# Optimization experiments

Measured on AMD Instinct MI355X. Metric: run time of the kernel, lower is better.

The kernel has to match this reference:

```python
import jax, jax.numpy as jnp
import numpy as np

NHEAD = 8
NEG_INF = -1e9
LN_EPS = 1e-5


def setup_inputs() -> dict:
    key = jax.random.key(0)
    ks = jax.random.split(key, 8)
    B, Q, N, C = 2, 256, 16384, 256
    return {
        "queries": jax.random.normal(ks[0], (B, Q, C), jnp.float32),
        "vid_features": jax.random.normal(ks[1], (B, C, N), jnp.float32),
        "vid_mask": jax.random.uniform(ks[2], (B, Q, N), jnp.float32),
        "pos_embed": jax.random.normal(ks[3], (B, C, N), jnp.float32),
        "query_embed": jax.random.normal(ks[4], (B, Q, C), jnp.float32),
        "in_proj_w": jax.random.normal(ks[5], (3 * C, C), jnp.float32) * 0.02,
        "in_proj_b": jnp.zeros((3 * C,), jnp.float32),
        "out_proj_w": jax.random.normal(ks[6], (C, C), jnp.float32) * 0.02,
        "out_proj_b": jnp.zeros((C,), jnp.float32),
        "ln_gamma": jnp.ones((C,), jnp.float32),
        "ln_beta": jnp.zeros((C,), jnp.float32),
    }


def reference(queries, vid_features, vid_mask, pos_embed, query_embed,
              in_proj_w, in_proj_b, out_proj_w, out_proj_b, ln_gamma, ln_beta):
    B, Q, C = queries.shape
    H = NHEAD
    d = C // H

    vf = jnp.transpose(vid_features, (0, 2, 1))   # B N C
    pe = jnp.transpose(pos_embed, (0, 2, 1))      # B N C

    q_in = queries + query_embed                  # with_pos_embed on queries
    k_in = vf + pe                                # with_pos_embed on keys
    v_in = vf

    wq, wk, wv = jnp.split(in_proj_w, 3, axis=0)
    bq, bk, bv = jnp.split(in_proj_b, 3)

    q = (q_in @ wq.T + bq).reshape(B, Q, H, d)
    k = (k_in @ wk.T + bk).reshape(B, -1, H, d)
    v = (v_in @ wv.T + bv).reshape(B, -1, H, d)

    scale = 1.0 / jnp.sqrt(jnp.asarray(d, q.dtype))
    logits = jnp.einsum('bqhd,bnhd->bhqn', q, k) * scale  # B H Q N

    # Hard masking: block keys where mask prob < 0.5; if a query row is
    # fully blocked, fall back to unmasked attention (avoid NaN softmax).
    blocked = vid_mask < 0.5                                 # B Q N
    all_blocked = jnp.all(blocked, axis=-1, keepdims=True)   # B Q 1
    blocked = blocked & jnp.logical_not(all_blocked)
    logits = jnp.where(blocked[:, None, :, :], NEG_INF, logits)

    attn = jax.nn.softmax(logits, axis=-1)
    ctx = jnp.einsum('bhqn,bnhd->bqhd', attn, v).reshape(B, Q, C)
    tgt2 = ctx @ out_proj_w.T + out_proj_b

    # residual + LayerNorm (dropout p=0.0 -> identity)
    x = queries + tgt2
    mu = jnp.mean(x, axis=-1, keepdims=True)
    var = jnp.mean(jnp.square(x - mu), axis=-1, keepdims=True)
    return (x - mu) / jnp.sqrt(var + LN_EPS) * ln_gamma + ln_beta
```

## Files before the change

kernel.cpp:

```cpp
#include <hip/hip_runtime.h>
#include <stdint.h>

#define B_ 2
#define Q_ 256
#define N_ 16384
#define C_ 256
#define H_ 8
#define D_ 32
#define NC_ 32
#define SCALEQ 0.2550542176432015f

typedef __bf16 bf16x8 __attribute__((ext_vector_type(8)));
typedef float f32x4 __attribute__((ext_vector_type(4)));

__device__ __forceinline__ uint16_t bfbits(float f) {
  union { __bf16 h; uint16_t u; } c; c.h = (__bf16)f; return c.u;
}
__device__ __forceinline__ float bf2f(uint16_t u) {
  union { uint32_t u; float f; } c; c.u = (uint32_t)u << 16;
  return c.f;
}
__device__ __forceinline__ uint32_t pk2(float a, float b) {
  union { struct { uint16_t lo, hi; } s; uint32_t u; } c;
  c.s.lo = bfbits(a); c.s.hi = bfbits(b);
  return c.u;
}
__device__ __forceinline__ void lgkm0_barrier() {
  __builtin_amdgcn_sched_barrier(0);
  asm volatile("s_waitcnt lgkmcnt(0)" ::: "memory");
  __builtin_amdgcn_sched_barrier(0);
  __builtin_amdgcn_s_barrier();
  __builtin_amdgcn_sched_barrier(0);
}

__global__ __launch_bounds__(256) void prep(const float* __restrict__ inw,
                                            const float* __restrict__ outw,
                                            const float* __restrict__ vm,
                                            uint16_t* __restrict__ wb,
                                            float* __restrict__ woT,
                                            uint32_t* __restrict__ mb) {
  __shared__ __align__(16) char sh[4352];
  const int bid = blockIdx.x;
  const int t = threadIdx.x;
  if (bid < 96) {
    const int i = (bid * 256 + t) * 8;
    const float4 a = *reinterpret_cast<const float4*>(inw + i);
    const float4 b = *reinterpret_cast<const float4*>(inw + i + 4);
    ushort4 lo = {bfbits(a.x), bfbits(a.y), bfbits(a.z), bfbits(a.w)};
    ushort4 hi = {bfbits(b.x), bfbits(b.y), bfbits(b.z), bfbits(b.w)};
    *reinterpret_cast<ushort4*>(wb + i) = lo;
    *reinterpret_cast<ushort4*>(wb + i + 4) = hi;
  } else if (bid < 160) {
    float(*s)[33] = reinterpret_cast<float(*)[33]>(sh);
    const int bb = bid - 96;
    const int bx = bb & 7, by = bb >> 3;
    const int r0 = by * 32, c0 = bx * 32;
    const int tr = t >> 5, tc = t & 31;
#pragma unroll
    for (int k = 0; k < 4; ++k)
      s[tr + 8 * k][tc] = outw[(size_t)(r0 + tr + 8 * k) * 256 + c0 + tc];
    __syncthreads();
#pragma unroll
    for (int k = 0; k < 4; ++k)
      woT[(size_t)(c0 + tr + 8 * k) * 256 + r0 + tc] = s[tc][tr + 8 * k];
  } else {
    uint8_t(*nib)[256] = reinterpret_cast<uint8_t(*)[256]>(sh);
    __shared__ int wcnt[4];
    __shared__ int tot;
    const int bq = bid - 160;
    const float* row = vm + (size_t)bq * N_;
    const int lane = t & 63;
    int cnt = 0;
#pragma unroll
    for (int i = 0; i < 16; ++i) {
      const float4 v = *reinterpret_cast<const float4*>(&row[i * 1024 + 4 * t]);
      const uint32_t nb = (v.x < 0.5f ? 1u : 0u) | (v.y < 0.5f ? 2u : 0u) |
                          (v.z < 0.5f ? 4u : 0u) | (v.w < 0.5f ? 8u : 0u);
      nib[i][t] = (uint8_t)nb;
      cnt += __popc(nb);
    }
    for (int o = 32; o > 0; o >>= 1) cnt += __shfl_down(cnt, o, 64);
    if (lane == 0) wcnt[t >> 6] = cnt;
    __syncthreads();
    if (t == 0) tot = wcnt[0] + wcnt[1] + wcnt[2] + wcnt[3];
    __syncthreads();
    const bool allb = (tot == N_);
    uint32_t* dst = mb + (size_t)bq * 512;
#pragma unroll
    for (int k = 0; k < 2; ++k) {
      const int w = k * 256 + t;
      const int i = w >> 5, tw = w & 31;
      const uint2 u = *reinterpret_cast<const uint2*>(&nib[i][8 * tw]);
      uint32_t y0 = u.x & 0x0F0F0F0Fu; y0 = y0 | (y0 >> 4);
      uint32_t y1 = u.y & 0x0F0F0F0Fu; y1 = y1 | (y1 >> 4);
      const uint32_t word = (y0 & 0xFFu) | (((y0 >> 16) & 0xFFu) << 8) |
                            ((y1 & 0xFFu) << 16) | (((y1 >> 16) & 0xFFu) << 24);
      dst[w] = allb ? 0u : word;
    }
  }
}

__global__ __launch_bounds__(512, 2) void kvqproj(const float* __restrict__ vf,
                                                  const float* __restrict__ pe,
                                                  const float* __restrict__ queries,
                                                  const float* __restrict__ qembed,
                                                  const uint16_t* __restrict__ wkv,
                                                  const float* __restrict__ bias,
                                                  uint16_t* __restrict__ Kh,
                                                  uint16_t* __restrict__ Vh,
                                                  uint16_t* __restrict__ Qb) {
  __shared__ __align__(16) uint16_t shpool[8][64][40];
  const int bid = blockIdx.x;
  const int t = threadIdx.x, wid = t >> 6, lane = t & 63;
  const int g = lane >> 4, c15 = lane & 15;

  if (bid >= 8) {
    const int kb = bid - 8;
    const int b = kb >> 8, nt = kb & 255;
    const int n0 = nt * 64;
    const int w = wid;

    const uint16_t* WsecK = wkv + (size_t)(256 + w * 32 + c15) * C_;
    const uint16_t* WsecV = wkv + (size_t)(512 + w * 32 + c15) * C_;

    f32x4 acck[8];
    f32x4 accv[8];
#pragma unroll
    for (int cf = 0; cf < 2; ++cf) {
      f32x4 ivk;
#pragma unroll
      for (int j = 0; j < 4; ++j) ivk[j] = bias[256 + w * 32 + cf * 16 + 4 * g + j];
      const float bv = bias[512 + w * 32 + cf * 16 + c15];
      const f32x4 ivv = {bv, bv, bv, bv};
#pragma unroll
      for (int nf = 0; nf < 4; ++nf) {
        acck[cf * 4 + nf] = ivk;
        accv[nf * 2 + cf] = ivv;
      }
    }

    const int cq = t >> 5, q2 = t & 31;
    const float* Xb = vf + ((size_t)b * C_ + 2 * cq) * N_ + n0 + 2 * q2;
    const float* Pb = pe + ((size_t)b * C_ + 2 * cq) * N_ + n0 + 2 * q2;
    const int cqs = cq ^ (((q2 >> 2) & 3) << 2);

    float2 xA0, xA1, pA0, pA1, xB0, xB1, pB0, pB1;
    bf16x8 Wk[2], Wv[2];

#define LOADW(s)                                                             \
    {                                                                        \
      _Pragma("unroll") for (int cf = 0; cf < 2; ++cf) {                     \
        Wk[cf] = *(const bf16x8*)(WsecK + (size_t)cf * 16 * C_ + (s) * 32 + g * 8); \
        Wv[cf] = *(const bf16x8*)(WsecV + (size_t)cf * 16 * C_ + (s) * 32 + g * 8); \
      }                                                                      \
    }
#define LOADA(X0, X1, P0, P1, s)                                             \
    {                                                                        \
      const float* x_ = Xb + (size_t)(s) * 32 * N_;                          \
      const float* p_ = Pb + (size_t)(s) * 32 * N_;                          \
      X0 = *(const float2*)x_;                                               \
      X1 = *(const float2*)(x_ + N_);                                        \
      P0 = *(const float2*)p_;                                               \
      P1 = *(const float2*)(p_ + N_);                                        \
    }
#define WRITEA(X0, X1, P0, P1, bufp)                                         \
    {                                                                        \
      *(uint32_t*)&shpool[bufp][2 * q2][2 * cqs]     = pk2(X0.x + P0.x, X1.x + P1.x); \
      *(uint32_t*)&shpool[bufp][2 * q2 + 1][2 * cqs] = pk2(X0.y + P0.y, X1.y + P1.y); \
      *(uint32_t*)&shpool[(bufp) + 1][2 * q2][2 * cqs]     = pk2(X0.x, X1.x); \
      *(uint32_t*)&shpool[(bufp) + 1][2 * q2 + 1][2 * cqs] = pk2(X0.y, X1.y); \
    }
#define COMPUTE(bufp)                                                        \
    {                                                                        \
      _Pragma("unroll") for (int nf = 0; nf < 4; ++nf) {                     \
        const int r_ = nf * 16 + c15;                                        \
        const int o_ = (g ^ ((r_ >> 3) & 3)) * 8;                            \
        const bf16x8 Fp = *(const bf16x8*)&shpool[bufp][r_][o_];             \
        const bf16x8 Fv = *(const bf16x8*)&shpool[(bufp) + 1][r_][o_];       \
        _Pragma("unroll") for (int cf = 0; cf < 2; ++cf) {                   \
          acck[cf * 4 + nf] = __builtin_amdgcn_mfma_f32_16x16x32_bf16(       \
              Wk[cf], Fp, acck[cf * 4 + nf], 0, 0, 0);                       \
          accv[nf * 2 + cf] = __builtin_amdgcn_mfma_f32_16x16x32_bf16(       \
              Fv, Wv[cf], accv[nf * 2 + cf], 0, 0, 0);                       \
        }                                                                    \
      }                                                                      \
    }

    LOADA(xA0, xA1, pA0, pA1, 0);
    LOADA(xB0, xB1, pB0, pB1, 1);
    LOADW(0); WRITEA(xA0, xA1, pA0, pA1, 0); LOADA(xA0, xA1, pA0, pA1, 2);
    lgkm0_barrier(); COMPUTE(0); __builtin_amdgcn_sched_barrier(0);
    LOADW(1); WRITEA(xB0, xB1, pB0, pB1, 2); LOADA(xB0, xB1, pB0, pB1, 3);
    lgkm0_barrier(); COMPUTE(2); __builtin_amdgcn_sched_barrier(0);
    LOADW(2); WRITEA(xA0, xA1, pA0, pA1, 0); LOADA(xA0, xA1, pA0, pA1, 4);
    lgkm0_barrier(); COMPUTE(0); __builtin_amdgcn_sched_barrier(0);
    LOADW(3); WRITEA(xB0, xB1, pB0, pB1, 2); LOADA(xB0, xB1, pB0, pB1, 5);
    lgkm0_barrier(); COMPUTE(2); __builtin_amdgcn_sched_barrier(0);
    LOADW(4); WRITEA(xA0, xA1, pA0, pA1, 0); LOADA(xA0, xA1, pA0, pA1, 6);
    lgkm0_barrier(); COMPUTE(0); __builtin_amdgcn_sched_barrier(0);
    LOADW(5); WRITEA(xB0, xB1, pB0, pB1, 2); LOADA(xB0, xB1, pB0, pB1, 7);
    lgkm0_barrier(); COMPUTE(2); __builtin_amdgcn_sched_barrier(0);
    LOADW(6); WRITEA(xA0, xA1, pA0, pA1, 0);
    lgkm0_barrier(); COMPUTE(0); __builtin_amdgcn_sched_barrier(0);
    LOADW(7); WRITEA(xB0, xB1, pB0, pB1, 2);
    lgkm0_barrier(); COMPUTE(2); __builtin_amdgcn_sched_barrier(0);

#undef LOADW
#undef LOADA
#undef WRITEA
#undef COMPUTE

    uint16_t* Kp = Kh + (size_t)(b * H_ + w) * N_ * D_;
#pragma unroll
    for (int cf = 0; cf < 2; ++cf)
#pragma unroll
      for (int nf = 0; nf < 4; ++nf) {
        const f32x4 a = acck[cf * 4 + nf];
        uint2 pkv;
        pkv.x = pk2(a[0], a[1]);
        pkv.y = pk2(a[2], a[3]);
        *(uint2*)&Kp[(size_t)(n0 + nf * 16 + c15) * D_ + cf * 16 + 4 * g] = pkv;
      }
    uint16_t* Vp = Vh + (size_t)(b * H_ + w) * D_ * N_;
#pragma unroll
    for (int nf = 0; nf < 4; ++nf)
#pragma unroll
      for (int cf = 0; cf < 2; ++cf) {
        const f32x4 a = accv[nf * 2 + cf];
        uint2 pkv;
        pkv.x = pk2(a[0], a[1]);
        pkv.y = pk2(a[2], a[3]);
        *(uint2*)&Vp[(size_t)(cf * 16 + c15) * N_ + n0 + nf * 16 + 4 * g] = pkv;
      }
  } else {
    const int qb = bid;
    const int q0g = qb * 64;
    const int b = q0g >> 8, q0 = q0g & 255;
    const int r = t >> 3, c0 = (t & 7) * 32, s = t & 7;
    const float* Qrow = queries + (size_t)(q0g + r) * C_ + c0;
    const float* Erow = qembed + (size_t)(q0g + r) * C_ + c0;
#pragma unroll
    for (int ph = 0; ph < 2; ++ph) {
      float4 a4[4], e4[4];
#pragma unroll
      for (int k = 0; k < 4; ++k) a4[k] = reinterpret_cast<const float4*>(Qrow + ph * 16)[k];
#pragma unroll
      for (int k = 0; k < 4; ++k) e4[k] = reinterpret_cast<const float4*>(Erow + ph * 16)[k];
      const float* af = reinterpret_cast<const float*>(a4);
      const float* ef = reinterpret_cast<const float*>(e4);
#pragma unroll
      for (int i = 0; i < 16; ++i) {
        const int cl = ph * 16 + i;
        const int col = cl ^ (8 * ((r >> 3) & 3));
        shpool[s][r][col] = bfbits(af[i] + ef[i]);
      }
      __builtin_amdgcn_sched_barrier(0);
    }
    lgkm0_barrier();

    const int w = wid;
    f32x4 acc[4][2];
#pragma unroll
    for (int nf = 0; nf < 2; ++nf) {
      const float bv = bias[w * 32 + nf * 16 + c15];
      const f32x4 iv = {bv, bv, bv, bv};
#pragma unroll
      for (int qf = 0; qf < 4; ++qf) acc[qf][nf] = iv;
    }
#pragma unroll
    for (int s8 = 0; s8 < 8; ++s8) {
      bf16x8 Bf[2];
#pragma unroll
      for (int nf = 0; nf < 2; ++nf)
        Bf[nf] = *reinterpret_cast<const bf16x8*>(
            wkv + (size_t)(w * 32 + nf * 16 + c15) * C_ + s8 * 32 + g * 8);
#pragma unroll
      for (int qf = 0; qf < 4; ++qf) {
        const int rr = qf * 16 + c15;
        const bf16x8 Af = *reinterpret_cast<const bf16x8*>(
            &shpool[s8][rr][8 * (g ^ ((rr >> 3) & 3))]);
#pragma unroll
        for (int nf = 0; nf < 2; ++nf)
          acc[qf][nf] = __builtin_amdgcn_mfma_f32_16x16x32_bf16(Af, Bf[nf], acc[qf][nf], 0, 0, 0);
      }
    }
#pragma unroll
    for (int qf = 0; qf < 4; ++qf)
#pragma unroll
      for (int nf = 0; nf < 2; ++nf)
#pragma unroll
        for (int j = 0; j < 4; ++j) {
          const int q = q0 + qf * 16 + 4 * g + j;
          const int dk = nf * 16 + c15;
          Qb[((size_t)(b * H_ + w) * Q_ + q) * D_ + dk] = bfbits(acc[qf][nf][j] * SCALEQ);
        }
  }
}

__global__ __launch_bounds__(512) void attn(const uint16_t* __restrict__ Qb,
                                            const uint16_t* __restrict__ Kh,
                                            const uint16_t* __restrict__ Vh,
                                            const uint32_t* __restrict__ mb,
                                            uint16_t* __restrict__ ctx_part,
                                            float* __restrict__ lsum_part) {
  const int bid = blockIdx.x;
  const int nc = bid & 31, h = (bid >> 5) & 7, b = bid >> 8;
  const int t = threadIdx.x, wid = t >> 6, lane = t & 63;
  const int g = lane >> 4, c15 = lane & 15;
  const int qw0 = wid * 32;
  const int nbase = nc * (N_ / NC_);
  constexpr int SS = (N_ / NC_) / 128;

  __shared__ __align__(16) uint16_t kst[2][128][40];
  __shared__ __align__(16) uint16_t vst[2][32][136];
  __shared__ __align__(16) uint16_t plds[8][32][40];

  const uint16_t* Qp = Qb + (size_t)(b * H_ + h) * Q_ * D_;
  bf16x8 qfr[2];
#pragma unroll
  for (int qf = 0; qf < 2; ++qf)
    qfr[qf] = *reinterpret_cast<const bf16x8*>(Qp + (size_t)(qw0 + qf * 16 + c15) * D_ + g * 8);

  f32x4 acc[2][2];
  const f32x4 zero4 = {0.f, 0.f, 0.f, 0.f};
#pragma unroll
  for (int qf = 0; qf < 2; ++qf)
#pragma unroll
    for (int dvf = 0; dvf < 2; ++dvf) acc[qf][dvf] = zero4;
  float lsum[2][4] = {};

  const uint32_t* mrow = mb + (size_t)b * Q_ * (N_ / 32);

  const int krow = t >> 2, kch = t & 3;
  const uint16_t* ksrc = Kh + ((size_t)(b * H_ + h) * N_ + nbase + krow) * 32 + kch * 8;
  const int vrow = t >> 4, vch = t & 15;
  const uint16_t* vsrc = Vh + ((size_t)(b * H_ + h) * 32 + vrow) * N_ + nbase + vch * 8;

  uint4 kreg = *(const uint4*)ksrc;
  uint4 vreg = *(const uint4*)vsrc;

  int cur = 0;
  for (int ss = 0; ss < SS; ++ss) {
    *(uint4*)&kst[cur][krow][kch * 8] = kreg;
    *(uint4*)&vst[cur][vrow][vch * 8] = vreg;
    if (ss < SS - 1) {
      kreg = *(const uint4*)(ksrc + (size_t)(ss + 1) * 128 * 32);
      vreg = *(const uint4*)(vsrc + (ss + 1) * 128);
    }
    lgkm0_barrier();

    const int nstart = nbase + ss * 128;
#pragma unroll
    for (int half = 0; half < 2; ++half) {
      uint32_t mw[2][4][2];
#pragma unroll
      for (int qf = 0; qf < 2; ++qf)
#pragma unroll
        for (int j = 0; j < 4; ++j) {
          const int q = qw0 + qf * 16 + 4 * g + j;
          const uint2 u = *reinterpret_cast<const uint2*>(
              &mrow[(size_t)q * (N_ / 32) + (nstart >> 5) + half * 2]);
          mw[qf][j][0] = u.x;
          mw[qf][j][1] = u.y;
        }
#pragma unroll
      for (int s2 = 0; s2 < 2; ++s2) {
        const int sub = half * 2 + s2;
        const int nl0 = sub * 32;
        bf16x8 kfr[2];
#pragma unroll
        for (int nf = 0; nf < 2; ++nf)
          kfr[nf] = *reinterpret_cast<const bf16x8*>(&kst[cur][nl0 + nf * 16 + c15][g * 8]);
        f32x4 s[2][2];
#pragma unroll
        for (int qf = 0; qf < 2; ++qf)
#pragma unroll
          for (int nf = 0; nf < 2; ++nf)
            s[qf][nf] = __builtin_amdgcn_mfma_f32_16x16x32_bf16(qfr[qf], kfr[nf], zero4, 0, 0, 0);

#pragma unroll
        for (int qf = 0; qf < 2; ++qf) {
#pragma unroll
          for (int j = 0; j < 4; ++j) {
            const uint32_t wmask = mw[qf][j][s2];
#pragma unroll
            for (int nf = 0; nf < 2; ++nf) {
              const int bit = nf * 16 + c15;
              const float p = ((wmask >> bit) & 1u) ? 0.0f : exp2f(s[qf][nf][j]);
              lsum[qf][j] += p;
              plds[wid][qf * 16 + 4 * g + j][nf * 16 + c15] = bfbits(p);
            }
          }
        }
        __asm__ volatile("s_waitcnt lgkmcnt(0)" ::: "memory");
#pragma unroll
        for (int qf = 0; qf < 2; ++qf) {
          const bf16x8 pa = *reinterpret_cast<const bf16x8*>(&plds[wid][qf * 16 + c15][g * 8]);
#pragma unroll
          for (int dvf = 0; dvf < 2; ++dvf) {
            const bf16x8 vb =
                *reinterpret_cast<const bf16x8*>(&vst[cur][dvf * 16 + c15][nl0 + g * 8]);
            acc[qf][dvf] = __builtin_amdgcn_mfma_f32_16x16x32_bf16(pa, vb, acc[qf][dvf], 0, 0, 0);
          }
        }
      }
    }
    __builtin_amdgcn_sched_barrier(0);
    cur ^= 1;
  }

#pragma unroll
  for (int qf = 0; qf < 2; ++qf)
#pragma unroll
    for (int j = 0; j < 4; ++j) {
      float v = lsum[qf][j];
      v += __shfl_xor(v, 1, 64);
      v += __shfl_xor(v, 2, 64);
      v += __shfl_xor(v, 4, 64);
      v += __shfl_xor(v, 8, 64);
      lsum[qf][j] = v;
    }

#pragma unroll
  for (int qf = 0; qf < 2; ++qf)
#pragma unroll
    for (int dvf = 0; dvf < 2; ++dvf)
#pragma unroll
      for (int j = 0; j < 4; ++j) {
        const int q = qw0 + qf * 16 + 4 * g + j;
        const size_t base = (((size_t)(b * Q_ + q) * H_ + h) * NC_ + nc) * D_;
        ctx_part[base + dvf * 16 + c15] = bfbits(acc[qf][dvf][j]);
      }
  if (c15 == 0) {
#pragma unroll
    for (int qf = 0; qf < 2; ++qf)
#pragma unroll
      for (int j = 0; j < 4; ++j) {
        const int q = qw0 + qf * 16 + 4 * g + j;
        lsum_part[((size_t)(b * Q_ + q) * H_ + h) * NC_ + nc] = lsum[qf][j];
      }
  }
}

__global__ __launch_bounds__(256) void epilogue(const uint16_t* __restrict__ ctx_part,
                                                const float* __restrict__ lsum_part,
                                                const float* __restrict__ queries,
                                                const float* __restrict__ woT,
                                                const float* __restrict__ bo,
                                                const float* __restrict__ gamma,
                                                const float* __restrict__ beta,
                                                float* __restrict__ out) {
  const int bq = blockIdx.x;
  const int t = threadIdx.x;
  const int h = t >> 5, dv = t & 31;
  const uint16_t* crow = ctx_part + (size_t)bq * H_ * NC_ * D_;
  const float* lrow = lsum_part + (size_t)bq * H_ * NC_;
  float cs = 0.f, ls = 0.f;
#pragma unroll 8
  for (int k = 0; k < NC_; ++k) {
    cs += bf2f(crow[((size_t)h * NC_ + k) * D_ + dv]);
    ls += lrow[h * NC_ + k];
  }
  __shared__ float ctxrow[C_];
  ctxrow[t] = cs / ls;
  __syncthreads();
  float acc = bo[t];
#pragma unroll 8
  for (int j = 0; j < C_; ++j) acc = fmaf(ctxrow[j], woT[(size_t)j * C_ + t], acc);
  const float x = queries[(size_t)bq * C_ + t] + acc;
  float s1 = x, s2 = x * x;
  for (int o = 32; o > 0; o >>= 1) {
    s1 += __shfl_down(s1, o, 64);
    s2 += __shfl_down(s2, o, 64);
  }
  __shared__ float r1[4], r2[4];
  if ((t & 63) == 0) { r1[t >> 6] = s1; r2[t >> 6] = s2; }
  __syncthreads();
  const float mu = (r1[0] + r1[1] + r1[2] + r1[3]) * (1.0f / C_);
  const float e2 = (r2[0] + r2[1] + r2[2] + r2[3]) * (1.0f / C_);
  const float var = e2 - mu * mu;
  out[(size_t)bq * C_ + t] = (x - mu) * rsqrtf(var + 1e-5f) * gamma[t] + beta[t];
}

extern "C" void kernel_launch(void* const* d_in, const int* in_sizes, int n_in,
                              void* d_out, int out_size, void* d_ws, size_t ws_size,
                              hipStream_t stream) {
  const float* queries    = (const float*)d_in[0];
  const float* vidfeat    = (const float*)d_in[1];
  const float* vidmask    = (const float*)d_in[2];
  const float* posembed   = (const float*)d_in[3];
  const float* queryembed = (const float*)d_in[4];
  const float* inw        = (const float*)d_in[5];
  const float* inb        = (const float*)d_in[6];
  const float* outw       = (const float*)d_in[7];
  const float* outb       = (const float*)d_in[8];
  const float* gamma      = (const float*)d_in[9];
  const float* beta       = (const float*)d_in[10];
  float* out = (float*)d_out;

  char* ws = (char*)d_ws;
  size_t off = 0;
  uint16_t* Qb   = (uint16_t*)(ws + off); off += (size_t)B_ * H_ * Q_ * D_ * 2;
  uint16_t* Kh   = (uint16_t*)(ws + off); off += (size_t)B_ * H_ * N_ * D_ * 2;
  uint16_t* Vh   = (uint16_t*)(ws + off); off += (size_t)B_ * H_ * D_ * N_ * 2;
  uint32_t* mb   = (uint32_t*)(ws + off); off += (size_t)B_ * Q_ * (N_ / 32) * 4;
  uint16_t* wkv  = (uint16_t*)(ws + off); off += (size_t)768 * C_ * 2;
  float* woT     = (float*)(ws + off);    off += (size_t)C_ * C_ * 4;
  uint16_t* ctxp = (uint16_t*)(ws + off); off += (size_t)B_ * Q_ * H_ * NC_ * D_ * 2;
  float* lsump   = (float*)(ws + off);    off += (size_t)B_ * Q_ * H_ * NC_ * 4;

  prep<<<dim3(672), dim3(256), 0, stream>>>(inw, outw, vidmask, wkv, woT, mb);
  kvqproj<<<dim3(520), dim3(512), 0, stream>>>(vidfeat, posembed, queries, queryembed,
                                               wkv, inb, Kh, Vh, Qb);
  attn<<<dim3(B_ * H_ * NC_), dim3(512), 0, stream>>>(Qb, Kh, Vh, mb, ctxp, lsump);
  epilogue<<<dim3(B_ * Q_), dim3(256), 0, stream>>>(ctxp, lsump, queries, woT, outb,
                                                    gamma, beta, out);
}
```

Baseline: 94.67 us.

## Split K and V projection across separate waves with 128-row tiles in 1024-thread blocks

The K/V projection block grows from 512 to 1024 threads and from 64 to 128 sequence rows. Waves 0-7 compute K and waves 8-15 compute V, so each wave holds one accumulator set and one weight fragment instead of both. The aim is to lower per-wave register pressure and to double the reuse of the staged activation tile. In exchange the grid shrinks to 264 blocks, which may under-fill the GPU, and half the threads sit idle in the Q-projection blocks.

```diff
diff --git a/kernel.cpp b/kernel.cpp
--- a/kernel.cpp
+++ b/kernel.cpp
@@ -100,59 +100,61 @@
   }
 }
 
-__global__ __launch_bounds__(512, 2) void kvqproj(const float* __restrict__ vf,
-                                                  const float* __restrict__ pe,
-                                                  const float* __restrict__ queries,
-                                                  const float* __restrict__ qembed,
-                                                  const uint16_t* __restrict__ wkv,
-                                                  const float* __restrict__ bias,
-                                                  uint16_t* __restrict__ Kh,
-                                                  uint16_t* __restrict__ Vh,
-                                                  uint16_t* __restrict__ Qb) {
-  __shared__ __align__(16) uint16_t shpool[8][64][40];
+__global__ __launch_bounds__(1024, 4) void kvqproj(const float* __restrict__ vf,
+                                                   const float* __restrict__ pe,
+                                                   const float* __restrict__ queries,
+                                                   const float* __restrict__ qembed,
+                                                   const uint16_t* __restrict__ wkv,
+                                                   const float* __restrict__ bias,
+                                                   uint16_t* __restrict__ Kh,
+                                                   uint16_t* __restrict__ Vh,
+                                                   uint16_t* __restrict__ Qb) {
+  __shared__ __align__(16) uint16_t shp[2][2][128][40];
   const int bid = blockIdx.x;
   const int t = threadIdx.x, wid = t >> 6, lane = t & 63;
   const int g = lane >> 4, c15 = lane & 15;
 
   if (bid >= 8) {
     const int kb = bid - 8;
-    const int b = kb >> 8, nt = kb & 255;
-    const int n0 = nt * 64;
-    const int w = wid;
-
-    const uint16_t* WsecK = wkv + (size_t)(256 + w * 32 + c15) * C_;
-    const uint16_t* WsecV = wkv + (size_t)(512 + w * 32 + c15) * C_;
-
-    f32x4 acck[8];
-    f32x4 accv[8];
-#pragma unroll
-    for (int cf = 0; cf < 2; ++cf) {
-      f32x4 ivk;
-#pragma unroll
-      for (int j = 0; j < 4; ++j) ivk[j] = bias[256 + w * 32 + cf * 16 + 4 * g + j];
-      const float bv = bias[512 + w * 32 + cf * 16 + c15];
-      const f32x4 ivv = {bv, bv, bv, bv};
-#pragma unroll
-      for (int nf = 0; nf < 4; ++nf) {
-        acck[cf * 4 + nf] = ivk;
-        accv[nf * 2 + cf] = ivv;
-      }
-    }
-
-    const int cq = t >> 5, q2 = t & 31;
-    const float* Xb = vf + ((size_t)b * C_ + 2 * cq) * N_ + n0 + 2 * q2;
-    const float* Pb = pe + ((size_t)b * C_ + 2 * cq) * N_ + n0 + 2 * q2;
-    const int cqs = cq ^ (((q2 >> 2) & 3) << 2);
+    const int b = kb >> 7, nt = kb & 127;
+    const int n0 = nt * 128;
+    const bool isK = wid < 8;
+    const int w = wid & 7;
+
+    const uint16_t* Wsec = wkv + (size_t)((isK ? 256 : 512) + w * 32 + c15) * C_;
+
+    f32x4 acc[16];
+    if (isK) {
+#pragma unroll
+      for (int cf = 0; cf < 2; ++cf) {
+        f32x4 iv;
+#pragma unroll
+        for (int j = 0; j < 4; ++j) iv[j] = bias[256 + w * 32 + cf * 16 + 4 * g + j];
+#pragma unroll
+        for (int nf = 0; nf < 8; ++nf) acc[cf * 8 + nf] = iv;
+      }
+    } else {
+#pragma unroll
+      for (int cf = 0; cf < 2; ++cf) {
+        const float bv = bias[512 + w * 32 + cf * 16 + c15];
+        const f32x4 iv = {bv, bv, bv, bv};
+#pragma unroll
+        for (int nf = 0; nf < 8; ++nf) acc[nf * 2 + cf] = iv;
+      }
+    }
+
+    const int cp = t >> 6, n2 = lane;
+    const float* Xb = vf + ((size_t)b * C_ + 2 * cp) * N_ + n0 + 2 * n2;
+    const float* Pb = pe + ((size_t)b * C_ + 2 * cp) * N_ + n0 + 2 * n2;
+    const int cps = cp ^ (((n2 >> 2) & 3) << 2);
 
     float2 xA0, xA1, pA0, pA1, xB0, xB1, pB0, pB1;
-    bf16x8 Wk[2], Wv[2];
+    bf16x8 W[2];
 
 #define LOADW(s)                                                             \
     {                                                                        \
-      _Pragma("unroll") for (int cf = 0; cf < 2; ++cf) {                     \
-        Wk[cf] = *(const bf16x8*)(WsecK + (size_t)cf * 16 * C_ + (s) * 32 + g * 8); \
-        Wv[cf] = *(const bf16x8*)(WsecV + (size_t)cf * 16 * C_ + (s) * 32 + g * 8); \
-      }                                                                      \
+      _Pragma("unroll") for (int cf = 0; cf < 2; ++cf)                       \
+          W[cf] = *(const bf16x8*)(Wsec + (size_t)cf * 16 * C_ + (s) * 32 + g * 8); \
     }
 #define LOADA(X0, X1, P0, P1, s)                                             \
     {                                                                        \
@@ -163,25 +165,28 @@
       P0 = *(const float2*)p_;                                               \
       P1 = *(const float2*)(p_ + N_);                                        \
     }
-#define WRITEA(X0, X1, P0, P1, bufp)                                         \
+#define WRITEA(X0, X1, P0, P1, buf)                                          \
     {                                                                        \
-      *(uint32_t*)&shpool[bufp][2 * q2][2 * cqs]     = pk2(X0.x + P0.x, X1.x + P1.x); \
-      *(uint32_t*)&shpool[bufp][2 * q2 + 1][2 * cqs] = pk2(X0.y + P0.y, X1.y + P1.y); \
-      *(uint32_t*)&shpool[(bufp) + 1][2 * q2][2 * cqs]     = pk2(X0.x, X1.x); \
-      *(uint32_t*)&shpool[(bufp) + 1][2 * q2 + 1][2 * cqs] = pk2(X0.y, X1.y); \
-    }
-#define COMPUTE(bufp)                                                        \
+      *(uint32_t*)&shp[0][buf][2 * n2][2 * cps]     = pk2(X0.x + P0.x, X1.x + P1.x); \
+      *(uint32_t*)&shp[0][buf][2 * n2 + 1][2 * cps] = pk2(X0.y + P0.y, X1.y + P1.y); \
+      *(uint32_t*)&shp[1][buf][2 * n2][2 * cps]     = pk2(X0.x, X1.x);       \
+      *(uint32_t*)&shp[1][buf][2 * n2 + 1][2 * cps] = pk2(X0.y, X1.y);       \
+    }
+#define COMPUTE(buf)                                                         \
     {                                                                        \
-      _Pragma("unroll") for (int nf = 0; nf < 4; ++nf) {                     \
+      _Pragma("unroll") for (int nf = 0; nf < 8; ++nf) {                     \
         const int r_ = nf * 16 + c15;                                        \
         const int o_ = (g ^ ((r_ >> 3) & 3)) * 8;                            \
-        const bf16x8 Fp = *(const bf16x8*)&shpool[bufp][r_][o_];             \
-        const bf16x8 Fv = *(const bf16x8*)&shpool[(bufp) + 1][r_][o_];       \
-        _Pragma("unroll") for (int cf = 0; cf < 2; ++cf) {                   \
-          acck[cf * 4 + nf] = __builtin_amdgcn_mfma_f32_16x16x32_bf16(       \
-              Wk[cf], Fp, acck[cf * 4 + nf], 0, 0, 0);                       \
-          accv[nf * 2 + cf] = __builtin_amdgcn_mfma_f32_16x16x32_bf16(       \
-              Fv, Wv[cf], accv[nf * 2 + cf], 0, 0, 0);                       \
+        if (isK) {                                                           \
+          const bf16x8 Fp = *(const bf16x8*)&shp[0][buf][r_][o_];            \
+          _Pragma("unroll") for (int cf = 0; cf < 2; ++cf)                   \
+              acc[cf * 8 + nf] = __builtin_amdgcn_mfma_f32_16x16x32_bf16(    \
+                  W[cf], Fp, acc[cf * 8 + nf], 0, 0, 0);                     \
+        } else {                                                             \
+          const bf16x8 Fv = *(const bf16x8*)&shp[1][buf][r_][o_];            \
+          _Pragma("unroll") for (int cf = 0; cf < 2; ++cf)                   \
+              acc[nf * 2 + cf] = __builtin_amdgcn_mfma_f32_16x16x32_bf16(    \
+                  Fv, W[cf], acc[nf * 2 + cf], 0, 0, 0);                     \
         }                                                                    \
       }                                                                      \
     }
@@ -190,110 +195,117 @@
     LOADA(xB0, xB1, pB0, pB1, 1);
     LOADW(0); WRITEA(xA0, xA1, pA0, pA1, 0); LOADA(xA0, xA1, pA0, pA1, 2);
     lgkm0_barrier(); COMPUTE(0); __builtin_amdgcn_sched_barrier(0);
-    LOADW(1); WRITEA(xB0, xB1, pB0, pB1, 2); LOADA(xB0, xB1, pB0, pB1, 3);
-    lgkm0_barrier(); COMPUTE(2); __builtin_amdgcn_sched_barrier(0);
+    LOADW(1); WRITEA(xB0, xB1, pB0, pB1, 1); LOADA(xB0, xB1, pB0, pB1, 3);
+    lgkm0_barrier(); COMPUTE(1); __builtin_amdgcn_sched_barrier(0);
     LOADW(2); WRITEA(xA0, xA1, pA0, pA1, 0); LOADA(xA0, xA1, pA0, pA1, 4);
     lgkm0_barrier(); COMPUTE(0); __builtin_amdgcn_sched_barrier(0);
-    LOADW(3); WRITEA(xB0, xB1, pB0, pB1, 2); LOADA(xB0, xB1, pB0, pB1, 5);
-    lgkm0_barrier(); COMPUTE(2); __builtin_amdgcn_sched_barrier(0);
+    LOADW(3); WRITEA(xB0, xB1, pB0, pB1, 1); LOADA(xB0, xB1, pB0, pB1, 5);
+    lgkm0_barrier(); COMPUTE(1); __builtin_amdgcn_sched_barrier(0);
     LOADW(4); WRITEA(xA0, xA1, pA0, pA1, 0); LOADA(xA0, xA1, pA0, pA1, 6);
     lgkm0_barrier(); COMPUTE(0); __builtin_amdgcn_sched_barrier(0);
-    LOADW(5); WRITEA(xB0, xB1, pB0, pB1, 2); LOADA(xB0, xB1, pB0, pB1, 7);
-    lgkm0_barrier(); COMPUTE(2); __builtin_amdgcn_sched_barrier(0);
+    LOADW(5); WRITEA(xB0, xB1, pB0, pB1, 1); LOADA(xB0, xB1, pB0, pB1, 7);
+    lgkm0_barrier(); COMPUTE(1); __builtin_amdgcn_sched_barrier(0);
     LOADW(6); WRITEA(xA0, xA1, pA0, pA1, 0);
     lgkm0_barrier(); COMPUTE(0); __builtin_amdgcn_sched_barrier(0);
-    LOADW(7); WRITEA(xB0, xB1, pB0, pB1, 2);
-    lgkm0_barrier(); COMPUTE(2); __builtin_amdgcn_sched_barrier(0);
+    LOADW(7); WRITEA(xB0, xB1, pB0, pB1, 1);
+    lgkm0_barrier(); COMPUTE(1); __builtin_amdgcn_sched_barrier(0);
 
 #undef LOADW
 #undef LOADA
 #undef WRITEA
 #undef COMPUTE
 
-    uint16_t* Kp = Kh + (size_t)(b * H_ + w) * N_ * D_;
-#pragma unroll
-    for (int cf = 0; cf < 2; ++cf)
-#pragma unroll
-      for (int nf = 0; nf < 4; ++nf) {
-        const f32x4 a = acck[cf * 4 + nf];
-        uint2 pkv;
-        pkv.x = pk2(a[0], a[1]);
-        pkv.y = pk2(a[2], a[3]);
-        *(uint2*)&Kp[(size_t)(n0 + nf * 16 + c15) * D_ + cf * 16 + 4 * g] = pkv;
-      }
-    uint16_t* Vp = Vh + (size_t)(b * H_ + w) * D_ * N_;
-#pragma unroll
-    for (int nf = 0; nf < 4; ++nf)
-#pragma unroll
-      for (int cf = 0; cf < 2; ++cf) {
-        const f32x4 a = accv[nf * 2 + cf];
-        uint2 pkv;
-        pkv.x = pk2(a[0], a[1]);
-        pkv.y = pk2(a[2], a[3]);
-        *(uint2*)&Vp[(size_t)(cf * 16 + c15) * N_ + n0 + nf * 16 + 4 * g] = pkv;
-      }
+    if (isK) {
+      uint16_t* Kp = Kh + (size_t)(b * H_ + w) * N_ * D_;
+#pragma unroll
+      for (int cf = 0; cf < 2; ++cf)
+#pragma unroll
+        for (int nf = 0; nf < 8; ++nf) {
+          const f32x4 a = acc[cf * 8 + nf];
+          uint2 pkv;
+          pkv.x = pk2(a[0], a[1]);
+          pkv.y = pk2(a[2], a[3]);
+          *(uint2*)&Kp[(size_t)(n0 + nf * 16 + c15) * D_ + cf * 16 + 4 * g] = pkv;
+        }
+    } else {
+      uint16_t* Vp = Vh + (size_t)(b * H_ + w) * D_ * N_;
+#pragma unroll
+      for (int nf = 0; nf < 8; ++nf)
+#pragma unroll
+        for (int cf = 0; cf < 2; ++cf) {
+          const f32x4 a = acc[nf * 2 + cf];
+          uint2 pkv;
+          pkv.x = pk2(a[0], a[1]);
+          pkv.y = pk2(a[2], a[3]);
+          *(uint2*)&Vp[(size_t)(cf * 16 + c15) * N_ + n0 + nf * 16 + 4 * g] = pkv;
+        }
+    }
   } else {
+    uint16_t(*qv)[64][40] = reinterpret_cast<uint16_t(*)[64][40]>(&shp[0][0][0][0]);
     const int qb = bid;
     const int q0g = qb * 64;
     const int b = q0g >> 8, q0 = q0g & 255;
-    const int r = t >> 3, c0 = (t & 7) * 32, s = t & 7;
-    const float* Qrow = queries + (size_t)(q0g + r) * C_ + c0;
-    const float* Erow = qembed + (size_t)(q0g + r) * C_ + c0;
-#pragma unroll
-    for (int ph = 0; ph < 2; ++ph) {
-      float4 a4[4], e4[4];
-#pragma unroll
-      for (int k = 0; k < 4; ++k) a4[k] = reinterpret_cast<const float4*>(Qrow + ph * 16)[k];
-#pragma unroll
-      for (int k = 0; k < 4; ++k) e4[k] = reinterpret_cast<const float4*>(Erow + ph * 16)[k];
-      const float* af = reinterpret_cast<const float*>(a4);
-      const float* ef = reinterpret_cast<const float*>(e4);
-#pragma unroll
-      for (int i = 0; i < 16; ++i) {
-        const int cl = ph * 16 + i;
-        const int col = cl ^ (8 * ((r >> 3) & 3));
-        shpool[s][r][col] = bfbits(af[i] + ef[i]);
-      }
-      __builtin_amdgcn_sched_barrier(0);
+    if (t < 512) {
+      const int r = t >> 3, c0 = (t & 7) * 32, s = t & 7;
+      const float* Qrow = queries + (size_t)(q0g + r) * C_ + c0;
+      const float* Erow = qembed + (size_t)(q0g + r) * C_ + c0;
+#pragma unroll
+      for (int ph = 0; ph < 2; ++ph) {
+        float4 a4[4], e4[4];
+#pragma unroll
+        for (int k = 0; k < 4; ++k) a4[k] = reinterpret_cast<const float4*>(Qrow + ph * 16)[k];
+#pragma unroll
+        for (int k = 0; k < 4; ++k) e4[k] = reinterpret_cast<const float4*>(Erow + ph * 16)[k];
+        const float* af = reinterpret_cast<const float*>(a4);
+        const float* ef = reinterpret_cast<const float*>(e4);
+#pragma unroll
+        for (int i = 0; i < 16; ++i) {
+          const int cl = ph * 16 + i;
+          const int col = cl ^ (8 * ((r >> 3) & 3));
+          qv[s][r][col] = bfbits(af[i] + ef[i]);
+        }
+        __builtin_amdgcn_sched_barrier(0);
+      }
     }
     lgkm0_barrier();
-
-    const int w = wid;
-    f32x4 acc[4][2];
-#pragma unroll
-    for (int nf = 0; nf < 2; ++nf) {
-      const float bv = bias[w * 32 + nf * 16 + c15];
-      const f32x4 iv = {bv, bv, bv, bv};
-#pragma unroll
-      for (int qf = 0; qf < 4; ++qf) acc[qf][nf] = iv;
-    }
-#pragma unroll
-    for (int s8 = 0; s8 < 8; ++s8) {
-      bf16x8 Bf[2];
-#pragma unroll
-      for (int nf = 0; nf < 2; ++nf)
-        Bf[nf] = *reinterpret_cast<const bf16x8*>(
-            wkv + (size_t)(w * 32 + nf * 16 + c15) * C_ + s8 * 32 + g * 8);
-#pragma unroll
-      for (int qf = 0; qf < 4; ++qf) {
-        const int rr = qf * 16 + c15;
-        const bf16x8 Af = *reinterpret_cast<const bf16x8*>(
-            &shpool[s8][rr][8 * (g ^ ((rr >> 3) & 3))]);
+    if (t < 512) {
+      const int w = wid;
+      f32x4 acc[4][2];
+#pragma unroll
+      for (int nf = 0; nf < 2; ++nf) {
+        const float bv = bias[w * 32 + nf * 16 + c15];
+        const f32x4 iv = {bv, bv, bv, bv};
+#pragma unroll
+        for (int qf = 0; qf < 4; ++qf) acc[qf][nf] = iv;
+      }
+#pragma unroll
+      for (int s8 = 0; s8 < 8; ++s8) {
+        bf16x8 Bf[2];
 #pragma unroll
         for (int nf = 0; nf < 2; ++nf)
-          acc[qf][nf] = __builtin_amdgcn_mfma_f32_16x16x32_bf16(Af, Bf[nf], acc[qf][nf], 0, 0, 0);
-      }
-    }
-#pragma unroll
-    for (int qf = 0; qf < 4; ++qf)
-#pragma unroll
-      for (int nf = 0; nf < 2; ++nf)
-#pragma unroll
-        for (int j = 0; j < 4; ++j) {
-          const int q = q0 + qf * 16 + 4 * g + j;
-          const int dk = nf * 16 + c15;
-          Qb[((size_t)(b * H_ + w) * Q_ + q) * D_ + dk] = bfbits(acc[qf][nf][j] * SCALEQ);
-        }
+          Bf[nf] = *reinterpret_cast<const bf16x8*>(
+              wkv + (size_t)(w * 32 + nf * 16 + c15) * C_ + s8 * 32 + g * 8);
+#pragma unroll
+        for (int qf = 0; qf < 4; ++qf) {
+          const int rr = qf * 16 + c15;
+          const bf16x8 Af = *reinterpret_cast<const bf16x8*>(
+              &qv[s8][rr][8 * (g ^ ((rr >> 3) & 3))]);
+#pragma unroll
+          for (int nf = 0; nf < 2; ++nf)
+            acc[qf][nf] = __builtin_amdgcn_mfma_f32_16x16x32_bf16(Af, Bf[nf], acc[qf][nf], 0, 0, 0);
+        }
+      }
+#pragma unroll
+      for (int qf = 0; qf < 4; ++qf)
+#pragma unroll
+        for (int nf = 0; nf < 2; ++nf)
+#pragma unroll
+          for (int j = 0; j < 4; ++j) {
+            const int q = q0 + qf * 16 + 4 * g + j;
+            const int dk = nf * 16 + c15;
+            Qb[((size_t)(b * H_ + w) * Q_ + q) * D_ + dk] = bfbits(acc[qf][nf][j] * SCALEQ);
+          }
+    }
   }
 }
 
@@ -510,8 +522,8 @@
   float* lsump   = (float*)(ws + off);    off += (size_t)B_ * Q_ * H_ * NC_ * 4;
 
   prep<<<dim3(672), dim3(256), 0, stream>>>(inw, outw, vidmask, wkv, woT, mb);
-  kvqproj<<<dim3(520), dim3(512), 0, stream>>>(vidfeat, posembed, queries, queryembed,
-                                               wkv, inb, Kh, Vh, Qb);
+  kvqproj<<<dim3(264), dim3(1024), 0, stream>>>(vidfeat, posembed, queries, queryembed,
+                                                wkv, inb, Kh, Vh, Qb);
   attn<<<dim3(B_ * H_ * NC_), dim3(512), 0, stream>>>(Qb, Kh, Vh, mb, ctxp, lsump);
   epilogue<<<dim3(B_ * Q_), dim3(256), 0, stream>>>(ctxp, lsump, queries, woT, outb,
                                                     gamma, beta, out);
```

New measurement: 89.82 us (median of 2 runs). 5.1% less time.
